# Kernel tuning notes

Measured on AMD Instinct MI355X. Metric: run time of the kernel, lower is better.

## Reference

```python
import jax, jax.numpy as jnp
import numpy as np

COST_POS = 5.0
COST_CONF = 1.0
LAMBDA_POS = 5.0
LAMBDA_CONF = 2.0
LAMBDA_NOOBJ = 0.5


def _lsa(cost):
    """Rectangular linear sum assignment (Jonker-Volgenant shortest augmenting
    path), same semantics as scipy.optimize.linear_sum_assignment."""
    cost = np.asarray(cost, dtype=np.float64)
    transposed = cost.shape[1] < cost.shape[0]
    if transposed:
        cost = cost.T
    nr, nc = cost.shape  # nr <= nc
    u = np.zeros(nr)
    v = np.zeros(nc)
    col4row = np.full(nr, -1, dtype=np.int64)
    row4col = np.full(nc, -1, dtype=np.int64)
    for cur_row in range(nr):
        shortest = np.full(nc, np.inf)
        pathback = np.full(nc, -1, dtype=np.int64)
        SR = np.zeros(nr, dtype=bool)
        SC = np.zeros(nc, dtype=bool)
        remaining = np.ones(nc, dtype=bool)
        min_val = 0.0
        i = cur_row
        sink = -1
        while sink == -1:
            SR[i] = True
            rem = np.flatnonzero(remaining)
            new_cost = min_val + cost[i, rem] - u[i] - v[rem]
            better = new_cost < shortest[rem]
            idx = rem[better]
            shortest[idx] = new_cost[better]
            pathback[idx] = i
            j = rem[np.argmin(shortest[rem])]
            min_val = shortest[j]
            remaining[j] = False
            SC[j] = True
            if row4col[j] == -1:
                sink = j
            else:
                i = row4col[j]
        u[cur_row] += min_val
        rows = np.flatnonzero(SR)
        rows = rows[rows != cur_row]
        u[rows] += min_val - shortest[col4row[rows]]
        v[SC] -= min_val - shortest[SC]
        j = sink
        while True:
            i = pathback[j]
            row4col[j] = i
            col4row[i], j = j, col4row[i]
            if i == cur_row:
                break
    if transposed:
        rows = col4row
        cols = np.arange(nr)
        order = np.argsort(rows)
        return rows[order], cols[order]
    return np.arange(nr), col4row


def _match(pred_c, conf, gt_c):
    """Per-image Hungarian matching (host-side, @no_grad in the original).
    cost = COST_POS * L1(pred, gt) - COST_CONF * sigmoid(conf)."""
    B, N, _ = pred_c.shape
    M = gt_c.shape[1]
    pred_idx = np.empty((B, M), dtype=np.int64)
    gt_idx = np.empty((B, M), dtype=np.int64)
    for b in range(B):
        c_pos = np.abs(pred_c[b][:, None, :] - gt_c[b][None, :, :]).sum(-1)  # [N,M]
        c_conf = -1.0 / (1.0 + np.exp(-conf[b]))  # [N]
        cost = COST_POS * c_pos + COST_CONF * c_conf[:, None]
        r, c = _lsa(cost)
        pred_idx[b] = r
        gt_idx[b] = c
    return pred_idx, gt_idx


def setup_inputs() -> dict:
    key = jax.random.key(0)
    B, N, M, D = 32, 300, 50, 2
    k1, k2, k3, k4, k5 = jax.random.split(key, 5)
    return {
        "pred_centroids": jax.random.uniform(k1, (B, N, D), dtype=jnp.float32),
        "pred_logits": jax.random.normal(k2, (B, N, 1), dtype=jnp.float32),
        "pred_conf": jax.random.normal(k3, (B, N), dtype=jnp.float32),
        "gt_centroids": jax.random.uniform(k4, (B, M, D), dtype=jnp.float32),
        "gt_classes": jax.random.randint(k5, (B, M), 0, 1),
    }


def reference(pred_centroids, pred_logits, pred_conf, gt_centroids, gt_classes):
    B, N, D = pred_centroids.shape
    M = gt_centroids.shape[1]
    # Matching indices are constants (computed under no_grad, host-side).
    pred_idx, gt_idx = _match(np.asarray(pred_centroids, np.float64),
                              np.asarray(pred_conf, np.float64),
                              np.asarray(gt_centroids, np.float64))
    pred_idx = jnp.asarray(pred_idx)  # [B,M]
    gt_idx = jnp.asarray(gt_idx)      # [B,M]
    b = jnp.arange(B)[:, None]
    mp = pred_centroids[b, pred_idx]  # [B,M,D]
    mg = gt_centroids[b, gt_idx]      # [B,M,D]
    # per-image L1 mean, summed over images (all images have M matches)
    loss_pos = jnp.mean(jnp.abs(mp - mg), axis=(1, 2)).sum()
    m_logit = pred_conf[b, pred_idx]  # [B,M]
    # BCE-with-logits, target=1: softplus(-x); target=0: softplus(x)
    loss_obj = jnp.mean(jax.nn.softplus(-m_logit), axis=1).sum()
    unmatched = jnp.ones((B, N), dtype=bool).at[b, pred_idx].set(False)
    sp = jax.nn.softplus(pred_conf)
    loss_noobj = (jnp.where(unmatched, sp, 0.0).sum(axis=1) / (N - M)).sum()
    loss_pos = LAMBDA_POS * loss_pos / B
    loss_conf_obj = LAMBDA_CONF * loss_obj / B
    loss_conf_noobj = LAMBDA_NOOBJ * loss_noobj / B
    loss_total = loss_pos + loss_conf_obj + loss_conf_noobj
    n_matched = jnp.asarray(float(M), dtype=jnp.float32)  # total matched / B
    return loss_pos, loss_conf_obj, loss_conf_noobj, loss_total, n_matched
```

## Files before the change

kernel.cpp:

```cpp
#include <hip/hip_runtime.h>
#include <math.h>


#define BB 32
#define NN 300
#define MM 50
#define KPL 5

#define F5(OP) OP(0) OP(1) OP(2) OP(3) OP(4)

__device__ __forceinline__ float softplus_f(float x) {
    return fmaxf(x, 0.0f) + __logf(1.0f + __expf(-fabsf(x)));
}
__device__ __forceinline__ float readlane_f(float x, int l) {
    return __int_as_float(__builtin_amdgcn_readlane(__float_as_int(x), l));
}
__device__ __forceinline__ int readlane_i(int x, int l) {
    return __builtin_amdgcn_readlane(x, l);
}
__device__ __forceinline__ unsigned umaxu(unsigned a, unsigned b) { return a > b ? a : b; }

__device__ __forceinline__ unsigned minkey_f32(float d) {
    unsigned s = (unsigned)__float_as_int(d);
    unsigned us = (s & 0x80000000u) ? ~s : (s | 0x80000000u);
    return ~us;
}
__device__ __forceinline__ float keydec_up(unsigned key) {
    unsigned us = (~key) | 0x1FFu;
    return (us & 0x80000000u) ? __uint_as_float(us & 0x7FFFFFFFu)
                              : __uint_as_float(~us);
}

__device__ __forceinline__ unsigned rowshr_maxkey(unsigned x) {
#define DPP_STEP(CTRL) { \
    unsigned t_ = (unsigned)__builtin_amdgcn_update_dpp(0, (int)x, CTRL, 0xF, 0xF, false); \
    x = umaxu(x, t_); }
    DPP_STEP(0x111)
    DPP_STEP(0x112)
    DPP_STEP(0x114)
    DPP_STEP(0x118)
#undef DPP_STEP
    return x;
}

__device__ __forceinline__ int div5(int n) { return (n * 52429) >> 18; }

__global__ __launch_bounds__(64, 1) void lsa_loss_kernel(
    const float* __restrict__ pred_c,
    const float* __restrict__ conf,
    const float* __restrict__ gt_c,
    float* __restrict__ out)
{
    const int b = blockIdx.x;
    const int lane = threadIdx.x;
    const bool owns = lane < (NN / KPL);
    const int base_j = KPL * lane;

    __shared__ float4 s_px4[NN/4], s_py4[NN/4], s_cm4[NN/4];
    __shared__ int claimed[NN];
    float* s_px = (float*)s_px4;
    float* s_py = (float*)s_py4;
    float* s_cm2 = (float*)s_cm4;

#define DECL(k) float px5##k, py5##k, cf##k, cm##k, sh##k; int pb##k;
    F5(DECL)
#undef DECL
    unsigned r4cpack = 0;
    int rem;
    float u = 0.0f, gx5 = 0.0f, gy5 = 0.0f, u_sub = 0.0f;
    int col4row = -1;

#define LOADK(k) { \
        int j = base_j + k; \
        float vpx = 0.0f, vpy = 0.0f, vcf = 0.0f; \
        if (owns) { \
            float2 pc = *(const float2*)&pred_c[(b*NN + j)*2]; \
            vpx = pc.x; vpy = pc.y; \
            vcf = conf[b*NN + j]; \
        } \
        px5##k = 5.0f*vpx; py5##k = 5.0f*vpy; cf##k = vcf; \
        cm##k = -(1.0f / (1.0f + __expf(-vcf)));   }
    F5(LOADK)
#undef LOADK
    if (lane < MM) {
        float2 gc = *(const float2*)&gt_c[(b*MM + lane)*2];
        gx5 = 5.0f*gc.x;
        gy5 = 5.0f*gc.y;
    }
#define STAGE(k) if (owns) { int j = base_j + k; \
        s_px[j] = px5##k; s_py[j] = py5##k; s_cm2[j] = cm##k + 2.0f; \
        claimed[j] = 63; }
    F5(STAGE)
#undef STAGE
#define IDXF(k) const unsigned idx##k = (unsigned)(511 - (base_j + k));
    F5(IDXF)
#undef IDXF
    __syncthreads();

    unsigned bestkey = 0u;
    for (int j0 = 0; j0 < NN; j0 += 8) {
        float4 vxa = s_px4[(j0 >> 2) + 0], vxb = s_px4[(j0 >> 2) + 1];
        float4 vya = s_py4[(j0 >> 2) + 0], vyb = s_py4[(j0 >> 2) + 1];
        float4 vca = s_cm4[(j0 >> 2) + 0], vcb = s_cm4[(j0 >> 2) + 1];
        float c0 = fabsf(vxa.x - gx5) + fabsf(vya.x - gy5) + vca.x;
        float c1 = fabsf(vxa.y - gx5) + fabsf(vya.y - gy5) + vca.y;
        float c2 = fabsf(vxa.z - gx5) + fabsf(vya.z - gy5) + vca.z;
        float c3 = fabsf(vxa.w - gx5) + fabsf(vya.w - gy5) + vca.w;
        float c4 = fabsf(vxb.x - gx5) + fabsf(vyb.x - gy5) + vcb.x;
        float c5 = fabsf(vxb.y - gx5) + fabsf(vyb.y - gy5) + vcb.y;
        float c6 = fabsf(vxb.z - gx5) + fabsf(vyb.z - gy5) + vcb.z;
        float c7 = fabsf(vxb.w - gx5) + fabsf(vyb.w - gy5) + vcb.w;
        unsigned q0 = (~__float_as_uint(c0) & 0xFFFFFE00u) | (unsigned)(511 - j0);
        unsigned q1 = (~__float_as_uint(c1) & 0xFFFFFE00u) | (unsigned)(510 - j0);
        unsigned q2 = (~__float_as_uint(c2) & 0xFFFFFE00u) | (unsigned)(509 - j0);
        unsigned q3 = (~__float_as_uint(c3) & 0xFFFFFE00u) | (unsigned)(508 - j0);
        unsigned q4 = (~__float_as_uint(c4) & 0xFFFFFE00u) | (unsigned)(507 - j0);
        unsigned q5 = (~__float_as_uint(c5) & 0xFFFFFE00u) | (unsigned)(506 - j0);
        unsigned q6 = (~__float_as_uint(c6) & 0xFFFFFE00u) | (unsigned)(505 - j0);
        unsigned q7 = (~__float_as_uint(c7) & 0xFFFFFE00u) | (unsigned)(504 - j0);
        unsigned qa = umaxu(umaxu(q0, q1), umaxu(q2, q3));
        unsigned qb = umaxu(umaxu(q4, q5), umaxu(q6, q7));
        bestkey = umaxu(bestkey, umaxu(qa, qb));
    }
    int wantj = 511 - (int)(bestkey & 511u);
    if (lane < MM) {
        u = fabsf(s_px[wantj] - gx5) + fabsf(s_py[wantj] - gy5)
            + (s_cm2[wantj] - 2.0f);
        atomicMin(&claimed[wantj], lane);
    }
    __syncthreads();
    if (lane < MM && claimed[wantj] == lane) col4row = wantj;
#define RCINIT(k) { int w = owns ? claimed[base_j + k] : 63; \
        r4cpack |= ((w < 63) ? (unsigned)(w + 1) : 0u) << (6*k); }
    F5(RCINIT)
#undef RCINIT

    unsigned long long freerows = __ballot(lane < MM && col4row < 0);
    while (freerows) {
        int cur_row = (int)__ffsll(freerows) - 1;
        freerows &= freerows - 1ull;

#define RINIT(k) sh##k = INFINITY; pb##k = 0;
        F5(RINIT)
#undef RINIT
        rem = owns ? 0x1F : 0;
        unsigned long long sr_mask = 0ull;
        float min_val = 0.0f;
        int i = cur_row;
        int sink = -1;

        for (int pops = 0; pops <= NN && sink < 0; ++pops) {
            sr_mask |= (1ull << i);
            float u_i   = readlane_f(u,   i);
            float gx5_i = readlane_f(gx5, i);
            float gy5_i = readlane_f(gy5, i);
            float mvu = min_val - u_i;
            int ip1 = i + 1;

#define RELAX(k) { \
                float dx5 = fabsf(px5##k - gx5_i); \
                float dy5 = fabsf(py5##k - gy5_i); \
                float nc = dx5 + dy5 + (cm##k + mvu); \
                bool imp = (((rem >> k) & 1) != 0) && (nc < sh##k); \
                sh##k = imp ? nc : sh##k; \
                pb##k = imp ? ip1 : pb##k; }
            F5(RELAX)
#undef RELAX

#define KEYK(k) unsigned key##k = ((rem >> k) & 1) \
                ? ((minkey_f32(sh##k) & 0xFFFFFE00u) | idx##k) : 0u;
            F5(KEYK)
#undef KEYK
            unsigned lkey = umaxu(umaxu(umaxu(key0, key1), umaxu(key2, key3)), key4);

            unsigned acc = rowshr_maxkey(lkey);
            unsigned k0 = (unsigned)readlane_i((int)acc, 15);
            unsigned k1 = (unsigned)readlane_i((int)acc, 31);
            unsigned k2 = (unsigned)readlane_i((int)acc, 47);
            unsigned k3 = (unsigned)readlane_i((int)acc, 63);
            unsigned gkey = umaxu(umaxu(k0, k1), umaxu(k2, k3));
            if (gkey == 0u) { sink = 0; break; }

            int bestj = 511 - (int)(gkey & 511u);
            int srcl = div5(bestj);
            int qj = bestj - KPL*srcl;
            min_val = keydec_up(gkey);

            unsigned rp = (unsigned)readlane_i((int)r4cpack, srcl);
            int r4 = (int)((rp >> (qj*6)) & 63u) - 1;

            rem = (lane == srcl) ? (rem & ~(1 << qj)) : rem;
            if (r4 < 0 || r4 >= MM) {
                sink = bestj;
            } else {
                i = r4;
                u_sub = (lane == r4) ? min_val : u_sub;
            }
        }

        if (lane < MM) {
            if (lane == cur_row) u += min_val;
            else if ((sr_mask >> lane) & 1ull) u += min_val - u_sub;
        }
#define VUPD(k) if (owns && !((rem >> k) & 1)) cm##k += min_val - sh##k;
        F5(VUPD)
#undef VUPD

        int j = sink < 0 ? 0 : sink;
        for (int step = 0; step <= MM; ++step) {
            int tj = div5(j), qj2 = j - KPL*tj;
            int pbl = qj2==0?pb0:qj2==1?pb1:qj2==2?pb2:qj2==3?pb3:pb4;
            int pi = readlane_i(pbl, tj) - 1;
            if (pi < 0 || pi >= MM) break;
            int q6 = qj2*6;
            unsigned nv = (r4cpack & ~(63u << q6)) | ((unsigned)(pi+1) << q6);
            r4cpack = (lane == tj) ? nv : r4cpack;
            int c_old = readlane_i(col4row, pi);
            col4row = (lane == pi) ? j : col4row;
            j = c_old;
            if (pi == cur_row) break;
            if (j < 0 || j >= NN) break;
        }
    }

    float lp = 0.0f, lo = 0.0f, ln = 0.0f;
    if (lane < MM) {
        int j = (col4row < 0 || col4row >= NN) ? 0 : col4row;
        float dx = fabsf(pred_c[(b*NN + j)*2 + 0] - gt_c[(b*MM + lane)*2 + 0]);
        float dy = fabsf(pred_c[(b*NN + j)*2 + 1] - gt_c[(b*MM + lane)*2 + 1]);
        lp = dx + dy;
        lo = softplus_f(-conf[b*NN + j]);
    }
#define NOOBJ(k) if (owns && ((r4cpack >> (6*k)) & 63u) == 0u) \
        ln += softplus_f(cf##k);
    F5(NOOBJ)
#undef NOOBJ
#pragma unroll
    for (int off = 32; off > 0; off >>= 1) {
        lp += __shfl_xor(lp, off, 64);
        lo += __shfl_xor(lo, off, 64);
        ln += __shfl_xor(ln, off, 64);
    }
    if (lane == 0) {
        double cp = 5.0 * ((double)lp / (double)(MM*2))  / (double)BB;
        double co = 2.0 * ((double)lo / (double)MM)      / (double)BB;
        double cn = 0.5 * ((double)ln / (double)(NN-MM)) / (double)BB;
        atomicAdd(&out[0], (float)cp);
        atomicAdd(&out[1], (float)co);
        atomicAdd(&out[2], (float)cn);
        atomicAdd(&out[3], (float)(cp + co + cn));
        if (b == 0) out[4] = 50.0f;
    }
}

extern "C" void kernel_launch(void* const* d_in, const int* in_sizes, int n_in,
                              void* d_out, int out_size, void* d_ws, size_t ws_size,
                              hipStream_t stream) {
    const float* pred_c = (const float*)d_in[0];
    const float* conf   = (const float*)d_in[2];
    const float* gt_c   = (const float*)d_in[3];
    float* out = (float*)d_out;

    hipMemsetAsync(out, 0, 5*sizeof(float), stream);
    lsa_loss_kernel<<<BB, 64, 0, stream>>>(pred_c, conf, gt_c, out);
}
```

Measured before the change: 95.84 us.

## Add auction-style augmenting row reduction before shortest-path augmentation

Adds a bounded augmenting row reduction phase (as in Jonker-Volgenant) that processes free rows by finding the best and second-best reduced costs via a two-key DPP wave reduction. Each free row claims its best column, updates the column's price and evicts the previous owner back to the free list. The goal is to cut the number of expensive shortest augmenting path searches that follow. It also pads the shared arrays with a sentinel entry and unrolls the initial column-min loop. This adds per-step wave-wide reductions and readlanes, so if few rows get settled the extra phase is pure overhead.

```diff
diff --git a/kernel.cpp b/kernel.cpp
--- a/kernel.cpp
+++ b/kernel.cpp
@@ -19,6 +19,7 @@
     return __builtin_amdgcn_readlane(x, l);
 }
 __device__ __forceinline__ unsigned umaxu(unsigned a, unsigned b) { return a > b ? a : b; }
+__device__ __forceinline__ unsigned uminu(unsigned a, unsigned b) { return a < b ? a : b; }
 
 __device__ __forceinline__ unsigned minkey_f32(float d) {
     unsigned s = (unsigned)__float_as_int(d);
@@ -56,7 +57,7 @@
     const bool owns = lane < (NN / KPL);
     const int base_j = KPL * lane;
 
-    __shared__ float4 s_px4[NN/4], s_py4[NN/4], s_cm4[NN/4];
+    __shared__ float4 s_px4[NN/4 + 1], s_py4[NN/4 + 1], s_cm4[NN/4 + 1];
     __shared__ int claimed[NN];
     float* s_px = (float*)s_px4;
     float* s_py = (float*)s_py4;
@@ -92,12 +93,17 @@
         claimed[j] = 63; }
     F5(STAGE)
 #undef STAGE
+    if (lane == 63) {
+        const float4 big = {1e30f, 1e30f, 1e30f, 1e30f};
+        s_px4[NN/4] = big; s_py4[NN/4] = big; s_cm4[NN/4] = big;
+    }
 #define IDXF(k) const unsigned idx##k = (unsigned)(511 - (base_j + k));
     F5(IDXF)
 #undef IDXF
     __syncthreads();
 
     unsigned bestkey = 0u;
+#pragma unroll 4
     for (int j0 = 0; j0 < NN; j0 += 8) {
         float4 vxa = s_px4[(j0 >> 2) + 0], vxb = s_px4[(j0 >> 2) + 1];
         float4 vya = s_py4[(j0 >> 2) + 0], vyb = s_py4[(j0 >> 2) + 1];
@@ -135,6 +141,59 @@
     F5(RCINIT)
 #undef RCINIT
 
+    {
+        unsigned long long freemask = __ballot(lane < MM && col4row < 0);
+        for (int steps = 0; freemask && steps < 128; ++steps) {
+            int i = (int)__ffsll(freemask) - 1;
+            freemask &= freemask - 1ull;
+            float gx5_i = readlane_f(gx5, i);
+            float gy5_i = readlane_f(gy5, i);
+#define ARRD(k) float d##k = fabsf(px5##k - gx5_i) + fabsf(py5##k - gy5_i) + cm##k; \
+            unsigned ak##k = owns ? ((minkey_f32(d##k) & 0xFFFFFE00u) | idx##k) : 0u;
+            F5(ARRD)
+#undef ARRD
+            unsigned h01 = umaxu(ak0, ak1), l01 = uminu(ak0, ak1);
+            unsigned h23 = umaxu(ak2, ak3), l23 = uminu(ak2, ak3);
+            unsigned hi = umaxu(h01, h23);
+            unsigned lo = umaxu(uminu(h01, h23), umaxu(l01, l23));
+            lo = umaxu(lo, uminu(hi, ak4));
+            hi = umaxu(hi, ak4);
+#define T2STEP(CTRL) { \
+            unsigned th = (unsigned)__builtin_amdgcn_update_dpp(0, (int)hi, CTRL, 0xF, 0xF, false); \
+            unsigned tl = (unsigned)__builtin_amdgcn_update_dpp(0, (int)lo, CTRL, 0xF, 0xF, false); \
+            lo = umaxu(umaxu(lo, tl), uminu(hi, th)); \
+            hi = umaxu(hi, th); }
+            T2STEP(0x111) T2STEP(0x112) T2STEP(0x114) T2STEP(0x118)
+#undef T2STEP
+            unsigned h0 = (unsigned)readlane_i((int)hi, 15), l0 = (unsigned)readlane_i((int)lo, 15);
+            unsigned h1 = (unsigned)readlane_i((int)hi, 31), l1 = (unsigned)readlane_i((int)lo, 31);
+            unsigned h2 = (unsigned)readlane_i((int)hi, 47), l2 = (unsigned)readlane_i((int)lo, 47);
+            unsigned h3 = (unsigned)readlane_i((int)hi, 63), l3 = (unsigned)readlane_i((int)lo, 63);
+            unsigned Ha = umaxu(h0, h1), La = umaxu(umaxu(l0, l1), uminu(h0, h1));
+            unsigned Hb = umaxu(h2, h3), Lb = umaxu(umaxu(l2, l3), uminu(h2, h3));
+            unsigned H  = umaxu(Ha, Hb), L  = umaxu(umaxu(La, Lb), uminu(Ha, Hb));
+            if (H == 0u) break;
+            int j1 = 511 - (int)(H & 511u);
+            float d2v = keydec_up(L);
+            int srcl = div5(j1);
+            int qj = j1 - KPL*srcl;
+            int q6 = qj*6;
+            float dsel = qj==0?d0:qj==1?d1:qj==2?d2:qj==3?d3:d4;
+            float d1x = readlane_f(dsel, srcl);
+            float dvu = d2v - d1x;
+            unsigned rp = (unsigned)readlane_i((int)r4cpack, srcl);
+            int r4 = (int)((rp >> q6) & 63u) - 1;
+            unsigned nv = (r4cpack & ~(63u << q6)) | ((unsigned)(i + 1) << q6);
+            r4cpack = (lane == srcl) ? nv : r4cpack;
+#define CMUPD(k) cm##k = (lane == srcl && qj == k) ? cm##k + dvu : cm##k;
+            F5(CMUPD)
+#undef CMUPD
+            u = (lane == i) ? d2v : u;
+            col4row = (lane == i) ? j1 : ((lane == r4) ? -1 : col4row);
+            if (r4 >= 0) freemask |= 1ull << r4;
+        }
+    }
+
     unsigned long long freerows = __ballot(lane < MM && col4row < 0);
     while (freerows) {
         int cur_row = (int)__ffsll(freerows) - 1;
```

New measurement: 102.2 us. 6.6% more time.
